# Kernel optimization log

Measured on AMD Instinct MI355X. Metric: run time of the kernel, lower is better.

Reference implementation:

```python
import jax, jax.numpy as jnp
import numpy as np

N_JOINTS = 18

_RELATIVE_JOINT_MAP = np.array([[0,3,2,1,3,3,3,3,3,3,3,3,3,3,3,3,3,3],[3,0,2,3,1,1,3,3,3,3,2,3,2,2,2,3,3,3],[2,2,0,1,1,3,3,3,1,2,2,3,3,3,3,3,3,3],[1,3,1,0,2,3,3,3,2,3,3,3,3,3,3,3,3,3],[3,1,1,2,0,2,3,2,2,3,1,3,3,3,3,3,3,3],[3,1,3,3,2,0,3,3,3,3,3,3,1,1,1,3,3,3],[3,3,3,3,3,3,0,3,2,1,3,3,3,3,3,3,3,3],[3,3,3,3,2,3,3,0,2,3,1,1,3,3,3,2,2,2],[3,3,1,2,2,3,2,2,0,1,1,3,3,3,3,3,3,3],[3,3,2,3,3,3,1,3,1,0,2,3,3,3,3,3,3,3],[3,2,2,3,1,3,3,1,1,2,0,2,3,3,3,3,3,3],[3,3,3,3,3,3,3,1,3,3,2,0,3,3,3,1,1,1],[3,2,3,3,3,1,3,3,3,3,3,3,0,1,2,3,3,3],[3,2,3,3,3,1,3,3,3,3,3,3,1,0,2,3,3,3],[3,2,3,3,3,1,3,3,3,3,3,3,2,2,0,3,3,3],[3,3,3,3,3,3,3,2,3,3,3,1,3,3,3,0,1,2],[3,3,3,3,3,3,3,2,3,3,3,1,3,3,3,1,0,2],[3,3,3,3,3,3,3,2,3,3,3,1,3,3,3,2,2,0]], dtype=np.int32)

DIM = 512
HEADS = 8
DEPTH = DIM // HEADS  # 64
BATCH = 4096


def setup_inputs() -> dict:
    key = jax.random.key(0)
    ks = jax.random.split(key, 10)
    std = 0.02
    return {
        "k": jax.random.normal(ks[0], (BATCH, N_JOINTS, DIM), jnp.float32),
        "v": jax.random.normal(ks[1], (BATCH, N_JOINTS, DIM), jnp.float32),
        "q": jax.random.normal(ks[2], (BATCH, N_JOINTS, DIM), jnp.float32),
        "Wq": jax.random.normal(ks[3], (DIM, DIM), jnp.float32) * (DIM ** -0.5),
        "Wk": jax.random.normal(ks[4], (DIM, DIM), jnp.float32) * (DIM ** -0.5),
        "Wv": jax.random.normal(ks[5], (DIM, DIM), jnp.float32) * (DIM ** -0.5),
        "Wo": jax.random.normal(ks[6], (DIM, DIM), jnp.float32) * (DIM ** -0.5),
        "bo": jnp.zeros((DIM,), jnp.float32),
        "rel_k": jax.random.normal(ks[7], (4, DEPTH), jnp.float32) * std,
        "rel_v": jax.random.normal(ks[8], (4, DEPTH), jnp.float32) * std,
        "joint_map": jnp.asarray(_RELATIVE_JOINT_MAP),
    }


def reference(k, v, q, Wq, Wk, Wv, Wo, bo, rel_k, rel_v, joint_map):
    B, n, dim = q.shape
    h, d = HEADS, DEPTH
    scale = d ** -0.5

    def split_heads(x):  # [B, n, h*d] -> [B, h, n, d]
        return x.reshape(B, n, h, d).transpose(0, 2, 1, 3)

    qh = split_heads(q @ Wq)
    kh = split_heads(k @ Wk)
    vh = split_heads(v @ Wv)

    # gather relative position tables: [n, n, d]
    r_pos_k = rel_k[joint_map]
    r_pos_v = rel_v[joint_map]

    # relative bias sums over heads AND depth of K (faithful to original einsum)
    rel_bias = jnp.einsum('bhid,ijd->bij', kh, r_pos_k)  # [B, n, n]
    dots = (jnp.einsum('bhid,bhjd->bhij', qh, kh) + rel_bias[:, None, :, :]) * scale
    att = jax.nn.softmax(dots, axis=-1)  # [B, h, n, n]

    out = jnp.einsum('bhij,bhjd->bhid', att, vh) + jnp.einsum('bhij,ijd->bhid', att, r_pos_v)
    out = out.transpose(0, 2, 1, 3).reshape(B, n, dim)
    out = out @ Wo + bo
    return out, att
```

## Files before the change

### kernel.cpp

```cpp
#include <hip/hip_runtime.h>
#include <stdint.h>

#define BATCH 4096
#define NJ 18
#define DIMM 512
#define HEADS 8
#define DEPTH 64
#define MROWS (BATCH*NJ)
#define ATT_OFF ((size_t)MROWS*DIMM)

typedef float f32x4 __attribute__((ext_vector_type(4)));
typedef _Float16 f16_t;
typedef _Float16 f16x8 __attribute__((ext_vector_type(8)));

__device__ __forceinline__ void gl_lds16(const unsigned int* g, unsigned int* l) {
    __builtin_amdgcn_global_load_lds(g, l, 16, 0, 0);
}

__global__ __launch_bounds__(256) void convert_w_kernel(
    const float* __restrict__ W0, const float* __restrict__ W1,
    const float* __restrict__ W2, const float* __restrict__ W3,
    f16_t* __restrict__ T0, f16_t* __restrict__ T1,
    f16_t* __restrict__ T2, f16_t* __restrict__ T3)
{
    const float* W = blockIdx.z == 0 ? W0 : blockIdx.z == 1 ? W1 : blockIdx.z == 2 ? W2 : W3;
    f16_t* T       = blockIdx.z == 0 ? T0 : blockIdx.z == 1 ? T1 : blockIdx.z == 2 ? T2 : T3;
    __shared__ float ld[64][65];
    int k0 = blockIdx.y * 64, n0 = blockIdx.x * 64;
    int tid = threadIdx.x;
    #pragma unroll
    for (int it = 0; it < 16; ++it) {
        int idx = tid + it * 256;
        int kk = idx >> 6, nn = idx & 63;
        ld[kk][nn] = W[(size_t)(k0 + kk) * DIMM + n0 + nn];
    }
    __syncthreads();
    f16x8* T8 = (f16x8*)T;
    #pragma unroll
    for (int it = 0; it < 2; ++it) {
        int c = tid + it * 256;
        int nn = c >> 3, c8 = c & 7;
        int n = n0 + nn, k = k0 + c8 * 8;
        f16x8 val;
        #pragma unroll
        for (int e = 0; e < 8; ++e) val[e] = (f16_t)ld[c8 * 8 + e][nn];
        size_t vi = (size_t)((n >> 7) * 8 + (k >> 6)) * 1024
                  + (n & 127) * 8 + (((k >> 3) & 7) ^ (n & 7));
        T8[vi] = val;
    }
}

__global__ __launch_bounds__(512) void gemm_qkv_kernel(
    const float* __restrict__ A0, const float* __restrict__ A1,
    const float* __restrict__ A2,
    const f16_t* __restrict__ B0, const f16_t* __restrict__ B1,
    const f16_t* __restrict__ B2,
    f16_t* __restrict__ C0, f16_t* __restrict__ C1, f16_t* __restrict__ C2)
{
    const float* A  = blockIdx.z == 0 ? A0 : blockIdx.z == 1 ? A1 : A2;
    const f16_t* Bt = blockIdx.z == 0 ? B0 : blockIdx.z == 1 ? B1 : B2;
    f16_t* C        = blockIdx.z == 0 ? C0 : blockIdx.z == 1 ? C1 : C2;

    const int p = blockIdx.x + 2 * blockIdx.y;
    const int logical = (p & 7) * (1152 / 8) + (p >> 3);
    const int bn = (logical & 1) * 256;
    const int bm = (logical >> 1) * 128;

    __shared__ __align__(16) f16_t As[128 * 64];
    __shared__ __align__(16) f16_t Bs[2 * 128 * 64];

    const int tid = threadIdx.x;
    const int lane = tid & 63;
    const int wv = tid >> 6;
    const int wm = wv >> 2, wn = wv & 3;
    const int l15 = lane & 15, lg = lane >> 4;
    const int swz = (l15 & 7) << 4;
    const int koffb[2] = { (lg * 16) ^ swz, (lg * 16 + 64) ^ swz };

    f32x4 acc[4][4] = {};

    for (int ks = 0; ks < 8; ++ks) {
        __syncthreads();
        {
            const unsigned int* bt0 =
                (const unsigned int*)(Bt + (size_t)(((bn >> 7) + 0) * 8 + ks) * 8192);
            const unsigned int* bt1 =
                (const unsigned int*)(Bt + (size_t)(((bn >> 7) + 1) * 8 + ks) * 8192);
            unsigned int* bs = (unsigned int*)Bs;
            #pragma unroll
            for (int it = 0; it < 4; ++it) {
                int chunk = wv * 4 + it;
                const unsigned int* src =
                    (chunk < 16 ? bt0 : bt1) + (chunk & 15) * 256 + lane * 4;
                gl_lds16(src, bs + chunk * 256);
            }
        }
        {
            #pragma unroll
            for (int r = 0; r < 2; ++r) {
                int c = tid + r * 512;
                int row = c >> 3, kc = c & 7;
                const f32x4* p4 = (const f32x4*)(A + (size_t)(bm + row) * DIMM + ks * 64 + kc * 8);
                f32x4 a0 = p4[0], a1 = p4[1];
                f16x8 val;
                val[0] = (f16_t)a0[0]; val[1] = (f16_t)a0[1];
                val[2] = (f16_t)a0[2]; val[3] = (f16_t)a0[3];
                val[4] = (f16_t)a1[0]; val[5] = (f16_t)a1[1];
                val[6] = (f16_t)a1[2]; val[7] = (f16_t)a1[3];
                ((f16x8*)As)[row * 8 + (kc ^ (row & 7))] = val;
            }
        }
        __syncthreads();

        #pragma unroll
        for (int kk = 0; kk < 2; ++kk) {
            const int koff = koffb[kk];
            f16x8 af[4], bfr[4];
            #pragma unroll
            for (int mi = 0; mi < 4; ++mi) {
                int row = wm * 64 + mi * 16 + l15;
                af[mi] = *(const f16x8*)((const char*)As + row * 128 + koff);
            }
            #pragma unroll
            for (int ni = 0; ni < 4; ++ni) {
                int rn = wn * 64 + ni * 16 + l15;
                bfr[ni] = *(const f16x8*)((const char*)Bs
                            + (rn >> 7) * 16384 + (rn & 127) * 128 + koff);
            }
            #pragma unroll
            for (int mi = 0; mi < 4; ++mi)
                #pragma unroll
                for (int ni = 0; ni < 4; ++ni)
                    acc[mi][ni] = __builtin_amdgcn_mfma_f32_16x16x32_f16(
                        af[mi], bfr[ni], acc[mi][ni], 0, 0, 0);
        }
    }

    #pragma unroll
    for (int mi = 0; mi < 4; ++mi) {
        #pragma unroll
        for (int ni = 0; ni < 4; ++ni) {
            int col = bn + wn * 64 + ni * 16 + l15;
            int rowb = bm + wm * 64 + mi * 16 + lg * 4;
            f32x4 v = acc[mi][ni];
            #pragma unroll
            for (int r = 0; r < 4; ++r)
                C[(size_t)(rowb + r) * DIMM + col] = (f16_t)v[r];
        }
    }
}

__global__ __launch_bounds__(512) void gemm_out_kernel(
    const f16_t* __restrict__ Aimg, const f16_t* __restrict__ Bt,
    float* __restrict__ C, const float* __restrict__ bias)
{
    const int p = blockIdx.x + 2 * blockIdx.y;
    const int logical = (p & 7) * (1152 / 8) + (p >> 3);
    const int bn = (logical & 1) * 256;
    const int bm = (logical >> 1) * 128;

    __shared__ __align__(16) f16_t As[128 * 64];
    __shared__ __align__(16) f16_t Bs[2 * 128 * 64];

    const int tid = threadIdx.x;
    const int lane = tid & 63;
    const int wv = tid >> 6;
    const int wm = wv >> 2, wn = wv & 3;
    const int l15 = lane & 15, lg = lane >> 4;
    const int swz = (l15 & 7) << 4;
    const int koffb[2] = { (lg * 16) ^ swz, (lg * 16 + 64) ^ swz };

    f32x4 acc[4][4] = {};

    for (int ks = 0; ks < 8; ++ks) {
        __syncthreads();
        {
            const unsigned int* bt0 =
                (const unsigned int*)(Bt + (size_t)(((bn >> 7) + 0) * 8 + ks) * 8192);
            const unsigned int* bt1 =
                (const unsigned int*)(Bt + (size_t)(((bn >> 7) + 1) * 8 + ks) * 8192);
            unsigned int* bs = (unsigned int*)Bs;
            #pragma unroll
            for (int it = 0; it < 4; ++it) {
                int chunk = wv * 4 + it;
                const unsigned int* src =
                    (chunk < 16 ? bt0 : bt1) + (chunk & 15) * 256 + lane * 4;
                gl_lds16(src, bs + chunk * 256);
            }
        }
        {
            const unsigned int* atile =
                (const unsigned int*)(Aimg + (size_t)((bm >> 7) * 8 + ks) * 8192);
            unsigned int* as = (unsigned int*)As;
            #pragma unroll
            for (int it = 0; it < 2; ++it) {
                int chunk = wv * 2 + it;
                gl_lds16(atile + chunk * 256 + lane * 4, as + chunk * 256);
            }
        }
        __syncthreads();

        #pragma unroll
        for (int kk = 0; kk < 2; ++kk) {
            const int koff = koffb[kk];
            f16x8 af[4], bfr[4];
            #pragma unroll
            for (int mi = 0; mi < 4; ++mi) {
                int row = wm * 64 + mi * 16 + l15;
                af[mi] = *(const f16x8*)((const char*)As + row * 128 + koff);
            }
            #pragma unroll
            for (int ni = 0; ni < 4; ++ni) {
                int rn = wn * 64 + ni * 16 + l15;
                bfr[ni] = *(const f16x8*)((const char*)Bs
                            + (rn >> 7) * 16384 + (rn & 127) * 128 + koff);
            }
            #pragma unroll
            for (int mi = 0; mi < 4; ++mi)
                #pragma unroll
                for (int ni = 0; ni < 4; ++ni)
                    acc[mi][ni] = __builtin_amdgcn_mfma_f32_16x16x32_f16(
                        af[mi], bfr[ni], acc[mi][ni], 0, 0, 0);
        }
    }

    #pragma unroll
    for (int mi = 0; mi < 4; ++mi) {
        #pragma unroll
        for (int ni = 0; ni < 4; ++ni) {
            int col = bn + wn * 64 + ni * 16 + l15;
            int rowb = bm + wm * 64 + mi * 16 + lg * 4;
            f32x4 v = acc[mi][ni];
            float bv = bias[col];
            #pragma unroll
            for (int r = 0; r < 4; ++r)
                C[(size_t)(rowb + r) * DIMM + col] = v[r] + bv;
        }
    }
}

__global__ __launch_bounds__(256, 3) void attn_kernel(
    const f16_t* __restrict__ qh, const f16_t* __restrict__ kh,
    const f16_t* __restrict__ vh,
    const float* __restrict__ rel_k, const float* __restrict__ rel_v,
    const int* __restrict__ jmap,
    float* __restrict__ att_out, f16_t* __restrict__ ao)
{
    const int b = blockIdx.x;
    const int tid = threadIdx.x;
    __shared__ __align__(16) f16_t k_s[NJ * DIMM];
    __shared__ __align__(16) f16_t v_s[NJ * DIMM];
    __shared__ float relk_s[4 * DEPTH];
    __shared__ float relv_s[4 * DEPTH];
    __shared__ int map_s[NJ * NJ];
    __shared__ float ksum_s[NJ * DEPTH];
    __shared__ float t4_s[NJ * 4];

    const size_t base = (size_t)b * (NJ * DIMM);
    const uint4* kg = (const uint4*)(kh + base);
    const uint4* vg = (const uint4*)(vh + base);
    uint4* ks4 = (uint4*)k_s;
    uint4* vs4 = (uint4*)v_s;
    for (int c = tid; c < 2 * NJ * 64; c += 256) {
        int t = c / (NJ * 64);
        int e = c - t * (NJ * 64);
        int m = e & 63;
        int pos = (e & ~63) + (m & 56) + (((m & 7) + (m >> 3)) & 7);
        uint4 val = (t == 0 ? kg : vg)[e];
        (t == 0 ? ks4 : vs4)[pos] = val;
    }
    relk_s[tid & 255] = rel_k[tid & 255];
    relv_s[tid & 255] = rel_v[tid & 255];
    for (int e = tid; e < NJ * NJ; e += 256) map_s[e] = jmap[e];

    const int h = tid / NJ, i = tid - (tid / NJ) * NJ;
    const bool act = tid < HEADS * NJ;
    f16x8 qr[8];
    if (act) {
        const f16x8* qp = (const f16x8*)(qh + base + i * DIMM + h * DEPTH);
        #pragma unroll
        for (int t = 0; t < 8; ++t) qr[t] = qp[t];
    }
    __syncthreads();

    const f16x8* ks8 = (const f16x8*)k_s;
    const f16x8* vs8 = (const f16x8*)v_s;

    for (int e = tid; e < NJ * DEPTH; e += 256) {
        int ii = e >> 6, dd = e & 63;
        int tt = dd >> 3, d7 = dd & 7;
        float s = 0.f;
        #pragma unroll
        for (int hh = 0; hh < HEADS; ++hh)
            s += (float)k_s[((ii << 6) + (hh << 3) + ((tt + hh) & 7)) * 8 + d7];
        ksum_s[e] = s;
    }
    __syncthreads();
    if (tid < NJ * 4) {
        int ii = tid >> 2, c = tid & 3;
        float s = 0.f;
        #pragma unroll
        for (int dd = 0; dd < DEPTH; ++dd)
            s += ksum_s[ii * DEPTH + dd] * relk_s[c * DEPTH + dd];
        t4_s[tid] = s;
    }
    __syncthreads();

    if (!act) return;

    float att[NJ];
    float m = -1e30f;
    #pragma unroll
    for (int j = 0; j < NJ; ++j) {
        float s = 0.f;
        #pragma unroll
        for (int t = 0; t < 8; ++t) {
            f16x8 kv = ks8[(j << 6) + (h << 3) + ((t + h) & 7)];
            f16x8 a = qr[t];
            #pragma unroll
            for (int e = 0; e < 8; ++e) s += (float)a[e] * (float)kv[e];
        }
        s += t4_s[i * 4 + map_s[i * NJ + j]];
        s *= 0.125f;
        att[j] = s;
        m = fmaxf(m, s);
    }
    float sum = 0.f;
    #pragma unroll
    for (int j = 0; j < NJ; ++j) { att[j] = __expf(att[j] - m); sum += att[j]; }
    const float inv = 1.f / sum;
    float s4[4] = {0.f, 0.f, 0.f, 0.f};
    float* ap = att_out + (((size_t)b * HEADS + h) * NJ + i) * NJ;
    #pragma unroll
    for (int j = 0; j < NJ; ++j) {
        float a = att[j] * inv;
        att[j] = a;
        ap[j] = a;
        int c = map_s[i * NJ + j];
        s4[0] += (c == 0) ? a : 0.f;
        s4[1] += (c == 1) ? a : 0.f;
        s4[2] += (c == 2) ? a : 0.f;
        s4[3] += (c == 3) ? a : 0.f;
    }

    const size_t grow = (size_t)b * NJ + i;
    f16x8* aot = (f16x8*)ao + ((grow >> 7) * 8 + h) * 1024 + (grow & 127) * 8;
    const int rr7 = (int)(grow & 7);
    #pragma unroll
    for (int half = 0; half < 2; ++half) {
        float acc[32] = {};
        #pragma unroll
        for (int j = 0; j < NJ; ++j) {
            float a = att[j];
            #pragma unroll
            for (int t = 0; t < 4; ++t) {
                int tt = half * 4 + t;
                f16x8 vv = vs8[(j << 6) + (h << 3) + ((tt + h) & 7)];
                #pragma unroll
                for (int e = 0; e < 8; ++e) acc[t * 8 + e] += a * (float)vv[e];
            }
        }
        #pragma unroll
        for (int c = 0; c < 4; ++c) {
            float sc = s4[c];
            #pragma unroll
            for (int d = 0; d < 32; ++d)
                acc[d] += sc * relv_s[c * DEPTH + half * 32 + d];
        }
        #pragma unroll
        for (int t = 0; t < 4; ++t) {
            f16x8 res;
            #pragma unroll
            for (int e = 0; e < 8; ++e) res[e] = (f16_t)acc[t * 8 + e];
            aot[(half * 4 + t) ^ rr7] = res;
        }
    }
}

extern "C" void kernel_launch(void* const* d_in, const int* in_sizes, int n_in,
                              void* d_out, int out_size, void* d_ws, size_t ws_size,
                              hipStream_t stream) {
    (void)in_sizes; (void)n_in; (void)out_size; (void)ws_size;
    const float* k_in = (const float*)d_in[0];
    const float* v_in = (const float*)d_in[1];
    const float* q_in = (const float*)d_in[2];
    const float* Wq   = (const float*)d_in[3];
    const float* Wk   = (const float*)d_in[4];
    const float* Wv   = (const float*)d_in[5];
    const float* Wo   = (const float*)d_in[6];
    const float* bo   = (const float*)d_in[7];
    const float* relk = (const float*)d_in[8];
    const float* relv = (const float*)d_in[9];
    const int*   jmap = (const int*)d_in[10];

    char* ws = (char*)d_ws;
    const size_t WT = (size_t)DIMM * DIMM * sizeof(f16_t);
    f16_t* Tq = (f16_t*)(ws + 0 * WT);
    f16_t* Tk = (f16_t*)(ws + 1 * WT);
    f16_t* Tv = (f16_t*)(ws + 2 * WT);
    f16_t* To = (f16_t*)(ws + 3 * WT);
    const size_t PSZ = (size_t)MROWS * DIMM * sizeof(f16_t);
    f16_t* qh = (f16_t*)(ws + 4 * WT + 0 * PSZ);
    f16_t* kh = (f16_t*)(ws + 4 * WT + 1 * PSZ);
    f16_t* vh = (f16_t*)(ws + 4 * WT + 2 * PSZ);
    f16_t* ao = (f16_t*)(ws + 4 * WT + 3 * PSZ);

    float* outp = (float*)d_out;
    float* attp = outp + ATT_OFF;

    convert_w_kernel<<<dim3(8, 8, 4), 256, 0, stream>>>(
        Wq, Wk, Wv, Wo, Tq, Tk, Tv, To);

    gemm_qkv_kernel<<<dim3(2, MROWS / 128, 3), 512, 0, stream>>>(
        q_in, k_in, v_in, Tq, Tk, Tv, qh, kh, vh);

    attn_kernel<<<BATCH, 256, 0, stream>>>(qh, kh, vh, relk, relv, jmap, attp, ao);

    gemm_out_kernel<<<dim3(2, MROWS / 128), 512, 0, stream>>>(
        ao, To, outp, bo);
}
```

Before: 432.7 us.

## Double-buffer B tiles and prefetch A registers in QKV GEMM

Software-pipelines the QKV projection GEMM. The next k-step's B tile is staged into a second LDS buffer via global_load_lds, and the next A fp32 values are prefetched into registers while the current step's MFMAs run, using explicit vmcnt waits and scheduling barriers. This hides global load latency behind compute. In exchange it doubles B shared memory, adds register pressure from the prefetched A values, and relies on hand-set waitcnt values, with a single As buffer guarded by barriers.

```diff
diff --git a/kernel.cpp b/kernel.cpp
--- a/kernel.cpp
+++ b/kernel.cpp
@@ -16,6 +16,9 @@
 __device__ __forceinline__ void gl_lds16(const unsigned int* g, unsigned int* l) {
     __builtin_amdgcn_global_load_lds(g, l, 16, 0, 0);
 }
+#define SBAR()  do { __builtin_amdgcn_sched_barrier(0); \
+                     __builtin_amdgcn_s_barrier();      \
+                     __builtin_amdgcn_sched_barrier(0); } while (0)
 
 __global__ __launch_bounds__(256) void convert_w_kernel(
     const float* __restrict__ W0, const float* __restrict__ W1,
@@ -67,7 +70,7 @@
     const int bm = (logical >> 1) * 128;
 
     __shared__ __align__(16) f16_t As[128 * 64];
-    __shared__ __align__(16) f16_t Bs[2 * 128 * 64];
+    __shared__ __align__(16) f16_t Bs[2 * 2 * 128 * 64];
 
     const int tid = threadIdx.x;
     const int lane = tid & 63;
@@ -77,40 +80,66 @@
     const int swz = (l15 & 7) << 4;
     const int koffb[2] = { (lg * 16) ^ swz, (lg * 16 + 64) ^ swz };
 
+    const int kc = tid & 7;
+    const int rw0 = tid >> 3;
+    const float* arow0 = A + (size_t)(bm + rw0) * DIMM + kc * 8;
+    const float* arow1 = A + (size_t)(bm + rw0 + 64) * DIMM + kc * 8;
+    const int awz = kc ^ (rw0 & 7);
+
     f32x4 acc[4][4] = {};
-
+    f32x4 apre[4];
+
+    auto loadA = [&](int ks) {
+        const f32x4* p0 = (const f32x4*)(arow0 + ks * 64);
+        const f32x4* p1 = (const f32x4*)(arow1 + ks * 64);
+        apre[0] = p0[0]; apre[1] = p0[1];
+        apre[2] = p1[0]; apre[3] = p1[1];
+    };
+    auto stageB = [&](int ks, int buf) {
+        const unsigned int* bt0 =
+            (const unsigned int*)(Bt + (size_t)(((bn >> 7) + 0) * 8 + ks) * 8192);
+        const unsigned int* bt1 =
+            (const unsigned int*)(Bt + (size_t)(((bn >> 7) + 1) * 8 + ks) * 8192);
+        unsigned int* bs = (unsigned int*)Bs + buf * 8192;
+        #pragma unroll
+        for (int it = 0; it < 4; ++it) {
+            int chunk = wv * 4 + it;
+            const unsigned int* src =
+                (chunk < 16 ? bt0 : bt1) + (chunk & 15) * 256 + lane * 4;
+            gl_lds16(src, bs + chunk * 256);
+        }
+    };
+
+    loadA(0);
+    stageB(0, 0);
+
+    #pragma unroll
     for (int ks = 0; ks < 8; ++ks) {
-        __syncthreads();
+        const int buf = ks & 1;
+
         {
-            const unsigned int* bt0 =
-                (const unsigned int*)(Bt + (size_t)(((bn >> 7) + 0) * 8 + ks) * 8192);
-            const unsigned int* bt1 =
-                (const unsigned int*)(Bt + (size_t)(((bn >> 7) + 1) * 8 + ks) * 8192);
-            unsigned int* bs = (unsigned int*)Bs;
-            #pragma unroll
-            for (int it = 0; it < 4; ++it) {
-                int chunk = wv * 4 + it;
-                const unsigned int* src =
-                    (chunk < 16 ? bt0 : bt1) + (chunk & 15) * 256 + lane * 4;
-                gl_lds16(src, bs + chunk * 256);
-            }
-        }
-        {
-            #pragma unroll
-            for (int r = 0; r < 2; ++r) {
-                int c = tid + r * 512;
-                int row = c >> 3, kc = c & 7;
-                const f32x4* p4 = (const f32x4*)(A + (size_t)(bm + row) * DIMM + ks * 64 + kc * 8);
-                f32x4 a0 = p4[0], a1 = p4[1];
-                f16x8 val;
-                val[0] = (f16_t)a0[0]; val[1] = (f16_t)a0[1];
-                val[2] = (f16_t)a0[2]; val[3] = (f16_t)a0[3];
-                val[4] = (f16_t)a1[0]; val[5] = (f16_t)a1[1];
-                val[6] = (f16_t)a1[2]; val[7] = (f16_t)a1[3];
-                ((f16x8*)As)[row * 8 + (kc ^ (row & 7))] = val;
-            }
-        }
-        __syncthreads();
+            f32x4 a0 = apre[0], a1 = apre[1], a2 = apre[2], a3 = apre[3];
+            f16x8 v0, v1;
+            v0[0] = (f16_t)a0[0]; v0[1] = (f16_t)a0[1];
+            v0[2] = (f16_t)a0[2]; v0[3] = (f16_t)a0[3];
+            v0[4] = (f16_t)a1[0]; v0[5] = (f16_t)a1[1];
+            v0[6] = (f16_t)a1[2]; v0[7] = (f16_t)a1[3];
+            v1[0] = (f16_t)a2[0]; v1[1] = (f16_t)a2[1];
+            v1[2] = (f16_t)a2[2]; v1[3] = (f16_t)a2[3];
+            v1[4] = (f16_t)a3[0]; v1[5] = (f16_t)a3[1];
+            v1[6] = (f16_t)a3[2]; v1[7] = (f16_t)a3[3];
+            ((f16x8*)As)[rw0 * 8 + awz]        = v0;
+            ((f16x8*)As)[(rw0 + 64) * 8 + awz] = v1;
+        }
+
+        if (ks < 7) {
+            loadA(ks + 1);
+            stageB(ks + 1, buf ^ 1);
+            asm volatile("s_waitcnt vmcnt(8) lgkmcnt(0)" ::: "memory");
+        } else {
+            asm volatile("s_waitcnt vmcnt(0) lgkmcnt(0)" ::: "memory");
+        }
+        SBAR();
 
         #pragma unroll
         for (int kk = 0; kk < 2; ++kk) {
@@ -124,7 +153,7 @@
             #pragma unroll
             for (int ni = 0; ni < 4; ++ni) {
                 int rn = wn * 64 + ni * 16 + l15;
-                bfr[ni] = *(const f16x8*)((const char*)Bs
+                bfr[ni] = *(const f16x8*)((const char*)Bs + buf * 32768
                             + (rn >> 7) * 16384 + (rn & 127) * 128 + koff);
             }
             #pragma unroll
@@ -134,6 +163,8 @@
                     acc[mi][ni] = __builtin_amdgcn_mfma_f32_16x16x32_f16(
                         af[mi], bfr[ni], acc[mi][ni], 0, 0, 0);
         }
+
+        SBAR();
     }
 
     #pragma unroll
```

After: 479.8 us. 1.11x slower.
